# Kernel optimization log

Hardware: AMD Instinct MI355X
Metric: run time of the kernel (lower is better)

The kernel has to match this reference:

```python
import jax, jax.numpy as jnp
import numpy as np

B, T, E, H, V, D, C = 16384, 128, 32, 128, 30001, 128, 3


def setup_inputs() -> dict:
    key = jax.random.key(0)
    ks = jax.random.split(key, 8)
    tokens = jax.random.randint(ks[0], (B, T), 0, V, dtype=jnp.int32)
    emb = jax.random.normal(ks[1], (V, E), jnp.float32) * 0.05
    W = jax.random.normal(ks[2], (E, 3 * H), jnp.float32) * (1.0 / np.sqrt(E))
    U = jax.random.normal(ks[3], (H, 3 * H), jnp.float32) * (1.0 / np.sqrt(H))
    b = jnp.zeros((2, 3 * H), jnp.float32)  # [input_bias, recurrent_bias] (reset_after=True)
    W1 = jax.random.normal(ks[4], (H, D), jnp.float32) * (1.0 / np.sqrt(H))
    b1 = jnp.zeros((D,), jnp.float32)
    Wout = jax.random.normal(ks[5], (D, C), jnp.float32) * (1.0 / np.sqrt(D))
    bout = jnp.zeros((C,), jnp.float32)
    return {"tokens": tokens, "emb": emb, "W": W, "U": U, "b": b,
            "W1": W1, "b1": b1, "Wout": Wout, "bout": bout}


def _gru_masked(x, mask, W, U, b):
    # x: [B,T,E], mask: [B,T] bool. Keras GRU defaults: reset_after=True,
    # activation=tanh, recurrent_activation=sigmoid. Masked steps freeze state.
    xp = jnp.einsum('bte,eg->btg', x, W) + b[0]  # precompute input projections [B,T,3H]

    def step(h, inp):
        xg, m = inp                      # xg: [B,3H], m: [B]
        rec = h @ U + b[1]               # [B,3H]
        z = jax.nn.sigmoid(xg[:, :H] + rec[:, :H])
        r = jax.nn.sigmoid(xg[:, H:2 * H] + rec[:, H:2 * H])
        hh = jnp.tanh(xg[:, 2 * H:] + r * rec[:, 2 * H:])
        h_new = z * h + (1.0 - z) * hh
        h = jnp.where(m[:, None], h_new, h)
        return h, None

    h0 = jnp.zeros((x.shape[0], H), x.dtype)
    h, _ = jax.lax.scan(step, h0, (jnp.swapaxes(xp, 0, 1), jnp.swapaxes(mask, 0, 1)))
    return h


def reference(tokens, emb, W, U, b, W1, b1, Wout, bout):
    x = emb[tokens]                      # [B,T,E] embedding lookup
    mask = tokens != 0                   # mask_zero=True
    h = _gru_masked(x, mask, W, U, b)    # [B,H]
    d = h @ W1 + b1
    d = d * jax.nn.sigmoid(d)            # swish
    logits = d @ Wout + bout
    return jax.nn.softmax(logits, axis=-1)
```

## Files before the change

### kernel.cpp

```cpp
#include <hip/hip_runtime.h>
#include <hip/hip_fp16.h>

#define B_ 16384
#define T_ 128
#define E_ 32
#define H_ 128
#define G3_ 384
#define V_ 30001
#define D_ 128
#define C_ 3

#define LOG2E 1.44269504088896340736f

typedef _Float16 f16;
typedef f16 f16x4 __attribute__((ext_vector_type(4)));
typedef f16 f16x8 __attribute__((ext_vector_type(8)));
typedef float f32x4 __attribute__((ext_vector_type(4)));
typedef unsigned int u32;
typedef u32 u32x4 __attribute__((ext_vector_type(4)));

#define H0_OFF   0
#define H1_OFF   4096
#define TOK_OFF  8192
#define DBUF_OFF 16384
#define LDS_TOTAL 24832

__device__ __forceinline__ float frcp_(float x)  { return __builtin_amdgcn_rcpf(x); }
__device__ __forceinline__ float fexp2_(float x) { return __builtin_amdgcn_exp2f(x); }

#define K1_ROWS 8
__global__ __launch_bounds__(384) void embw_kernel(
    const float* __restrict__ emb,
    const float* __restrict__ W,
    const float* __restrict__ b_in,
    f16* __restrict__ embW)
{
    __shared__ float sW[E_][G3_];
    __shared__ float sE[K1_ROWS][E_];
    const int g = threadIdx.x;
    #pragma unroll
    for (int e = 0; e < E_; ++e) sW[e][g] = W[e * G3_ + g];
    const int v0 = blockIdx.x * K1_ROWS;
    for (int idx = g; idx < K1_ROWS * E_; idx += 384) {
        int rr = idx >> 5, ee = idx & 31;
        int v = v0 + rr;
        sE[rr][ee] = (v < V_) ? emb[v * E_ + ee] : 0.f;
    }
    __syncthreads();
    const float bg = b_in[g];
    const int c = g & 127, slot = g >> 7;
    const float sc = (slot == 2) ? (2.f * LOG2E) : (-LOG2E);
    #pragma unroll
    for (int rr = 0; rr < K1_ROWS; ++rr) {
        int v = v0 + rr;
        if (v >= V_) break;
        float acc = bg;
        #pragma unroll
        for (int e = 0; e < E_; ++e) acc = fmaf(sE[rr][e], sW[e][g], acc);
        embW[(size_t)v * 512 + c * 4 + slot] = (f16)(acc * sc);
    }
}

__global__ __launch_bounds__(512, 4) void gru_mfma_kernel(
    const int*   __restrict__ tokens,
    const f16*   __restrict__ embW,
    const float* __restrict__ U,
    const float* __restrict__ b,
    const float* __restrict__ W1,
    const float* __restrict__ b1,
    const float* __restrict__ Wout,
    const float* __restrict__ bout,
    float* __restrict__ out)
{
    __shared__ char lds[LDS_TOTAL];
    const int tid = threadIdx.x;
    const int w   = tid >> 6;
    const int l   = tid & 63;
    const int cl  = l & 15;
    const int q   = l >> 4;
    const int R0  = blockIdx.x * 16;
    const int col = w * 16 + cl;

    for (int idx = tid; idx < 16 * T_; idx += 512) {
        int r = idx >> 7, t = idx & 127;
        u32 tok = (u32)tokens[(size_t)(R0 + r) * T_ + t];
        *(u32*)(&lds[TOK_OFF + t * 64 + r * 4]) = tok * 1024u;
    }
    for (int idx = tid; idx < 1024; idx += 512)
        ((float*)(lds + H0_OFF))[idx] = 0.f;

    f16x8 Bf[3][4];
    #pragma unroll
    for (int gt = 0; gt < 3; ++gt) {
        const float sc = (gt == 2) ? (2.f * LOG2E) : (-LOG2E);
        const int n = gt * 128 + col;
        #pragma unroll
        for (int kt = 0; kt < 4; ++kt) {
            const int k0 = kt * 32 + q * 8;
            f16x8 fr;
            #pragma unroll
            for (int j = 0; j < 8; ++j)
                fr[j] = (f16)(U[(size_t)(k0 + j) * G3_ + n] * sc);
            Bf[gt][kt] = fr;
        }
    }

    const float bz = -LOG2E * b[G3_ + col];
    const float br = -LOG2E * b[G3_ + 128 + col];
    const float bh = 2.f * LOG2E * b[G3_ + 256 + col];

    float hreg[4];
    #pragma unroll
    for (int i = 0; i < 4; ++i) hreg[i] = 0.f;

    __syncthreads();

    const char* embWb = (const char*)embW;
    const int col8 = col * 8;

    u32x4 offc = *(const u32x4*)(&lds[TOK_OFF + q * 16]);
    f16x4 xvc[4];
    #pragma unroll
    for (int i = 0; i < 4; ++i)
        xvc[i] = *(const f16x4*)(embWb + offc[i] + col8);

    int cur = 0;
    for (int t = 0; t < T_; ++t) {
        const char* hb = lds + (cur ? H1_OFF : H0_OFF);
        char*       hn = lds + (cur ? H0_OFF : H1_OFF);

        u32x4 offn = offc;
        f16x4 xvn[4];
        #pragma unroll
        for (int i = 0; i < 4; ++i) xvn[i] = xvc[i];
        if (t + 1 < T_) {
            offn = *(const u32x4*)(&lds[TOK_OFF + (t + 1) * 64 + q * 16]);
            #pragma unroll
            for (int i = 0; i < 4; ++i)
                xvn[i] = *(const f16x4*)(embWb + offn[i] + col8);
        }

        f32x4 accz = {bz, bz, bz, bz};
        f32x4 accr = {br, br, br, br};
        f32x4 acch = {bh, bh, bh, bh};
        #pragma unroll
        for (int kt = 0; kt < 4; ++kt) {
            const int chunk = (kt * 64 + q * 16) ^ ((cl & 7) << 4);
            const f16x8 af = *(const f16x8*)(hb + cl * 256 + chunk);
            accz = __builtin_amdgcn_mfma_f32_16x16x32_f16(af, Bf[0][kt], accz, 0, 0, 0);
            accr = __builtin_amdgcn_mfma_f32_16x16x32_f16(af, Bf[1][kt], accr, 0, 0, 0);
            acch = __builtin_amdgcn_mfma_f32_16x16x32_f16(af, Bf[2][kt], acch, 0, 0, 0);
        }

        #pragma unroll
        for (int i = 0; i < 4; ++i) {
            const float z  = frcp_(1.f + fexp2_((float)xvc[i][0] + accz[i]));
            const float r  = frcp_(1.f + fexp2_((float)xvc[i][1] + accr[i]));
            const float hh = fmaf(-2.f, frcp_(1.f + fexp2_(fmaf(r, acch[i], (float)xvc[i][2]))), 1.f);
            const float hv = hreg[i];
            float nv = fmaf(z, hv - hh, hh);
            nv = (offc[i] != 0u) ? nv : hv;
            hreg[i] = nv;
            const int row = 4 * q + i;
            *(f16*)(hn + row * 256 + ((col * 2) ^ ((row & 7) << 4))) = (f16)nv;
        }
        __syncthreads();
        cur ^= 1;
        offc = offn;
        #pragma unroll
        for (int i = 0; i < 4; ++i) xvc[i] = xvn[i];
    }

    {
        f16x8 Wf[4];
        #pragma unroll
        for (int kt = 0; kt < 4; ++kt) {
            const int k0 = kt * 32 + q * 8;
            f16x8 fr;
            #pragma unroll
            for (int j = 0; j < 8; ++j)
                fr[j] = (f16)W1[(size_t)(k0 + j) * D_ + col];
            Wf[kt] = fr;
        }
        const char* hb = lds + H0_OFF;
        const float bd = b1[col];
        f32x4 dacc = {bd, bd, bd, bd};
        #pragma unroll
        for (int kt = 0; kt < 4; ++kt) {
            const int chunk = (kt * 64 + q * 16) ^ ((cl & 7) << 4);
            const f16x8 af = *(const f16x8*)(hb + cl * 256 + chunk);
            dacc = __builtin_amdgcn_mfma_f32_16x16x32_f16(af, Wf[kt], dacc, 0, 0, 0);
        }
        #pragma unroll
        for (int i = 0; i < 4; ++i) {
            const float v = dacc[i];
            const float sw = v * frcp_(1.f + fexp2_(-LOG2E * v));
            *(float*)(&lds[DBUF_OFF + (4 * q + i) * 528 + col * 4]) = sw;
        }
    }
    __syncthreads();

    if (w == 0 && l < 48) {
        const int row = l & 15, ci = l >> 4;
        float acc = bout[ci];
        #pragma unroll 4
        for (int k = 0; k < D_; ++k)
            acc = fmaf(*(const float*)(&lds[DBUF_OFF + row * 528 + k * 4]),
                       Wout[k * 3 + ci], acc);
        const float v0 = __shfl(acc, row);
        const float v1 = __shfl(acc, row + 16);
        const float v2 = __shfl(acc, row + 32);
        const float mx = fmaxf(v0, fmaxf(v1, v2));
        const float e0 = fexp2_(LOG2E * (v0 - mx));
        const float e1 = fexp2_(LOG2E * (v1 - mx));
        const float e2 = fexp2_(LOG2E * (v2 - mx));
        const float inv = frcp_(e0 + e1 + e2);
        const float mine = (ci == 0) ? e0 : (ci == 1) ? e1 : e2;
        out[(size_t)(R0 + row) * 3 + ci] = mine * inv;
    }
}

extern "C" void kernel_launch(void* const* d_in, const int* in_sizes, int n_in,
                              void* d_out, int out_size, void* d_ws, size_t ws_size,
                              hipStream_t stream) {
    (void)in_sizes; (void)n_in; (void)out_size; (void)ws_size;
    const int*   tokens = (const int*)d_in[0];
    const float* emb    = (const float*)d_in[1];
    const float* W      = (const float*)d_in[2];
    const float* U      = (const float*)d_in[3];
    const float* b      = (const float*)d_in[4];
    const float* W1     = (const float*)d_in[5];
    const float* b1     = (const float*)d_in[6];
    const float* Wout   = (const float*)d_in[7];
    const float* bout   = (const float*)d_in[8];
    float* out  = (float*)d_out;
    f16*   embW = (f16*)d_ws;

    hipLaunchKernelGGL(embw_kernel, dim3((V_ + K1_ROWS - 1) / K1_ROWS), dim3(384), 0, stream,
                       emb, W, b, embW);
    hipLaunchKernelGGL(gru_mfma_kernel, dim3(B_ / 16), dim3(512), 0, stream,
                       tokens, embW, U, b, W1, b1, Wout, bout, out);
}
```

Baseline: 375.7 us.

## Transpose recurrent MFMA so each lane owns one row with 4 contiguous columns

Swaps MFMA operand roles so U is the A operand and h is the B operand. Each lane then holds four consecutive hidden columns of a single batch row. This lets the mask come from one token per lane and lets the embedding projection be read as three contiguous f16x4 loads from a plain [V,384] layout. The hidden-state store becomes one f16x4 write per lane instead of four scalar f16 writes, and the XOR swizzle is replaced by a padded 272-byte row pitch. The per-step gather stays the same size, but it is now split into three separate 8-byte loads per lane, each at a different 256-byte offset.

```diff
diff --git a/kernel.cpp b/kernel.cpp
--- a/kernel.cpp
+++ b/kernel.cpp
@@ -17,13 +17,13 @@
 typedef f16 f16x8 __attribute__((ext_vector_type(8)));
 typedef float f32x4 __attribute__((ext_vector_type(4)));
 typedef unsigned int u32;
-typedef u32 u32x4 __attribute__((ext_vector_type(4)));
-
+
+#define HPITCH   272
 #define H0_OFF   0
-#define H1_OFF   4096
-#define TOK_OFF  8192
-#define DBUF_OFF 16384
-#define LDS_TOTAL 24832
+#define H1_OFF   4352
+#define TOK_OFF  8704
+#define DBUF_OFF 16896
+#define LDS_TOTAL 25344
 
 __device__ __forceinline__ float frcp_(float x)  { return __builtin_amdgcn_rcpf(x); }
 __device__ __forceinline__ float fexp2_(float x) { return __builtin_amdgcn_exp2f(x); }
@@ -48,8 +48,7 @@
     }
     __syncthreads();
     const float bg = b_in[g];
-    const int c = g & 127, slot = g >> 7;
-    const float sc = (slot == 2) ? (2.f * LOG2E) : (-LOG2E);
+    const float sc = (g >= 256) ? (2.f * LOG2E) : (-LOG2E);
     #pragma unroll
     for (int rr = 0; rr < K1_ROWS; ++rr) {
         int v = v0 + rr;
@@ -57,7 +56,7 @@
         float acc = bg;
         #pragma unroll
         for (int e = 0; e < E_; ++e) acc = fmaf(sE[rr][e], sW[e][g], acc);
-        embW[(size_t)v * 512 + c * 4 + slot] = (f16)(acc * sc);
+        embW[(size_t)v * G3_ + g] = (f16)(acc * sc);
     }
 }
 
@@ -79,21 +78,21 @@
     const int cl  = l & 15;
     const int q   = l >> 4;
     const int R0  = blockIdx.x * 16;
-    const int col = w * 16 + cl;
+    const int c0  = w * 16 + 4 * q;
 
     for (int idx = tid; idx < 16 * T_; idx += 512) {
         int r = idx >> 7, t = idx & 127;
         u32 tok = (u32)tokens[(size_t)(R0 + r) * T_ + t];
-        *(u32*)(&lds[TOK_OFF + t * 64 + r * 4]) = tok * 1024u;
-    }
-    for (int idx = tid; idx < 1024; idx += 512)
+        *(u32*)(&lds[TOK_OFF + t * 64 + r * 4]) = tok * 768u;
+    }
+    for (int idx = tid; idx < H1_OFF / 4; idx += 512)
         ((float*)(lds + H0_OFF))[idx] = 0.f;
 
-    f16x8 Bf[3][4];
+    f16x8 Af[3][4];
     #pragma unroll
     for (int gt = 0; gt < 3; ++gt) {
         const float sc = (gt == 2) ? (2.f * LOG2E) : (-LOG2E);
-        const int n = gt * 128 + col;
+        const int n = gt * 128 + w * 16 + cl;
         #pragma unroll
         for (int kt = 0; kt < 4; ++kt) {
             const int k0 = kt * 32 + q * 8;
@@ -101,13 +100,17 @@
             #pragma unroll
             for (int j = 0; j < 8; ++j)
                 fr[j] = (f16)(U[(size_t)(k0 + j) * G3_ + n] * sc);
-            Bf[gt][kt] = fr;
-        }
-    }
-
-    const float bz = -LOG2E * b[G3_ + col];
-    const float br = -LOG2E * b[G3_ + 128 + col];
-    const float bh = 2.f * LOG2E * b[G3_ + 256 + col];
+            Af[gt][kt] = fr;
+        }
+    }
+
+    f32x4 bz4, br4, bh4;
+    #pragma unroll
+    for (int i = 0; i < 4; ++i) {
+        bz4[i] = -LOG2E * b[G3_ + c0 + i];
+        br4[i] = -LOG2E * b[G3_ + 128 + c0 + i];
+        bh4[i] = 2.f * LOG2E * b[G3_ + 256 + c0 + i];
+    }
 
     float hreg[4];
     #pragma unroll
@@ -116,59 +119,61 @@
     __syncthreads();
 
     const char* embWb = (const char*)embW;
-    const int col8 = col * 8;
-
-    u32x4 offc = *(const u32x4*)(&lds[TOK_OFF + q * 16]);
-    f16x4 xvc[4];
-    #pragma unroll
-    for (int i = 0; i < 4; ++i)
-        xvc[i] = *(const f16x4*)(embWb + offc[i] + col8);
+    const int colb = c0 * 2;
+
+    u32 offc = *(const u32*)(&lds[TOK_OFF + cl * 4]);
+    f16x4 xzc = *(const f16x4*)(embWb + offc + colb);
+    f16x4 xrc = *(const f16x4*)(embWb + offc + colb + 256);
+    f16x4 xhc = *(const f16x4*)(embWb + offc + colb + 512);
 
     int cur = 0;
     for (int t = 0; t < T_; ++t) {
         const char* hb = lds + (cur ? H1_OFF : H0_OFF);
         char*       hn = lds + (cur ? H0_OFF : H1_OFF);
 
-        u32x4 offn = offc;
-        f16x4 xvn[4];
-        #pragma unroll
-        for (int i = 0; i < 4; ++i) xvn[i] = xvc[i];
+        u32 offn = offc;
+        f16x4 xzn = xzc, xrn = xrc, xhn = xhc;
         if (t + 1 < T_) {
-            offn = *(const u32x4*)(&lds[TOK_OFF + (t + 1) * 64 + q * 16]);
-            #pragma unroll
-            for (int i = 0; i < 4; ++i)
-                xvn[i] = *(const f16x4*)(embWb + offn[i] + col8);
-        }
-
-        f32x4 accz = {bz, bz, bz, bz};
-        f32x4 accr = {br, br, br, br};
-        f32x4 acch = {bh, bh, bh, bh};
-        #pragma unroll
-        for (int kt = 0; kt < 4; ++kt) {
-            const int chunk = (kt * 64 + q * 16) ^ ((cl & 7) << 4);
-            const f16x8 af = *(const f16x8*)(hb + cl * 256 + chunk);
-            accz = __builtin_amdgcn_mfma_f32_16x16x32_f16(af, Bf[0][kt], accz, 0, 0, 0);
-            accr = __builtin_amdgcn_mfma_f32_16x16x32_f16(af, Bf[1][kt], accr, 0, 0, 0);
-            acch = __builtin_amdgcn_mfma_f32_16x16x32_f16(af, Bf[2][kt], acch, 0, 0, 0);
-        }
-
+            offn = *(const u32*)(&lds[TOK_OFF + (t + 1) * 64 + cl * 4]);
+            xzn = *(const f16x4*)(embWb + offn + colb);
+            xrn = *(const f16x4*)(embWb + offn + colb + 256);
+            xhn = *(const f16x4*)(embWb + offn + colb + 512);
+        }
+
+        const f16x8 bf0 = *(const f16x8*)(hb + cl * HPITCH + q * 16);
+        const f16x8 bf1 = *(const f16x8*)(hb + cl * HPITCH + q * 16 + 64);
+        const f16x8 bf2 = *(const f16x8*)(hb + cl * HPITCH + q * 16 + 128);
+        const f16x8 bf3 = *(const f16x8*)(hb + cl * HPITCH + q * 16 + 192);
+        f32x4 accz = __builtin_amdgcn_mfma_f32_16x16x32_f16(Af[0][0], bf0, bz4, 0, 0, 0);
+        f32x4 accr = __builtin_amdgcn_mfma_f32_16x16x32_f16(Af[1][0], bf0, br4, 0, 0, 0);
+        f32x4 acch = __builtin_amdgcn_mfma_f32_16x16x32_f16(Af[2][0], bf0, bh4, 0, 0, 0);
+        accz = __builtin_amdgcn_mfma_f32_16x16x32_f16(Af[0][1], bf1, accz, 0, 0, 0);
+        accr = __builtin_amdgcn_mfma_f32_16x16x32_f16(Af[1][1], bf1, accr, 0, 0, 0);
+        acch = __builtin_amdgcn_mfma_f32_16x16x32_f16(Af[2][1], bf1, acch, 0, 0, 0);
+        accz = __builtin_amdgcn_mfma_f32_16x16x32_f16(Af[0][2], bf2, accz, 0, 0, 0);
+        accr = __builtin_amdgcn_mfma_f32_16x16x32_f16(Af[1][2], bf2, accr, 0, 0, 0);
+        acch = __builtin_amdgcn_mfma_f32_16x16x32_f16(Af[2][2], bf2, acch, 0, 0, 0);
+        accz = __builtin_amdgcn_mfma_f32_16x16x32_f16(Af[0][3], bf3, accz, 0, 0, 0);
+        accr = __builtin_amdgcn_mfma_f32_16x16x32_f16(Af[1][3], bf3, accr, 0, 0, 0);
+        acch = __builtin_amdgcn_mfma_f32_16x16x32_f16(Af[2][3], bf3, acch, 0, 0, 0);
+
+        f16x4 hv4;
         #pragma unroll
         for (int i = 0; i < 4; ++i) {
-            const float z  = frcp_(1.f + fexp2_((float)xvc[i][0] + accz[i]));
-            const float r  = frcp_(1.f + fexp2_((float)xvc[i][1] + accr[i]));
-            const float hh = fmaf(-2.f, frcp_(1.f + fexp2_(fmaf(r, acch[i], (float)xvc[i][2]))), 1.f);
+            const float z  = frcp_(1.f + fexp2_((float)xzc[i] + accz[i]));
+            const float r  = frcp_(1.f + fexp2_((float)xrc[i] + accr[i]));
+            const float hh = fmaf(-2.f, frcp_(1.f + fexp2_(fmaf(r, acch[i], (float)xhc[i]))), 1.f);
             const float hv = hreg[i];
             float nv = fmaf(z, hv - hh, hh);
-            nv = (offc[i] != 0u) ? nv : hv;
+            nv = (offc != 0u) ? nv : hv;
             hreg[i] = nv;
-            const int row = 4 * q + i;
-            *(f16*)(hn + row * 256 + ((col * 2) ^ ((row & 7) << 4))) = (f16)nv;
-        }
+            hv4[i] = (f16)nv;
+        }
+        *(f16x4*)(hn + cl * HPITCH + colb) = hv4;
+
         __syncthreads();
         cur ^= 1;
-        offc = offn;
-        #pragma unroll
-        for (int i = 0; i < 4; ++i) xvc[i] = xvn[i];
+        offc = offn; xzc = xzn; xrc = xrn; xhc = xhn;
     }
 
     {
@@ -179,24 +184,28 @@
             f16x8 fr;
             #pragma unroll
             for (int j = 0; j < 8; ++j)
-                fr[j] = (f16)W1[(size_t)(k0 + j) * D_ + col];
+                fr[j] = (f16)W1[(size_t)(k0 + j) * D_ + w * 16 + cl];
             Wf[kt] = fr;
         }
         const char* hb = lds + H0_OFF;
-        const float bd = b1[col];
-        f32x4 dacc = {bd, bd, bd, bd};
-        #pragma unroll
-        for (int kt = 0; kt < 4; ++kt) {
-            const int chunk = (kt * 64 + q * 16) ^ ((cl & 7) << 4);
-            const f16x8 af = *(const f16x8*)(hb + cl * 256 + chunk);
-            dacc = __builtin_amdgcn_mfma_f32_16x16x32_f16(af, Wf[kt], dacc, 0, 0, 0);
-        }
+        f32x4 bd4;
+        #pragma unroll
+        for (int i = 0; i < 4; ++i) bd4[i] = b1[c0 + i];
+        const f16x8 bf0 = *(const f16x8*)(hb + cl * HPITCH + q * 16);
+        const f16x8 bf1 = *(const f16x8*)(hb + cl * HPITCH + q * 16 + 64);
+        const f16x8 bf2 = *(const f16x8*)(hb + cl * HPITCH + q * 16 + 128);
+        const f16x8 bf3 = *(const f16x8*)(hb + cl * HPITCH + q * 16 + 192);
+        f32x4 dacc = __builtin_amdgcn_mfma_f32_16x16x32_f16(Wf[0], bf0, bd4, 0, 0, 0);
+        dacc = __builtin_amdgcn_mfma_f32_16x16x32_f16(Wf[1], bf1, dacc, 0, 0, 0);
+        dacc = __builtin_amdgcn_mfma_f32_16x16x32_f16(Wf[2], bf2, dacc, 0, 0, 0);
+        dacc = __builtin_amdgcn_mfma_f32_16x16x32_f16(Wf[3], bf3, dacc, 0, 0, 0);
+        f32x4 sw4;
         #pragma unroll
         for (int i = 0; i < 4; ++i) {
             const float v = dacc[i];
-            const float sw = v * frcp_(1.f + fexp2_(-LOG2E * v));
-            *(float*)(&lds[DBUF_OFF + (4 * q + i) * 528 + col * 4]) = sw;
-        }
+            sw4[i] = v * frcp_(1.f + fexp2_(-LOG2E * v));
+        }
+        *(f32x4*)(&lds[DBUF_OFF + cl * 528 + c0 * 4]) = sw4;
     }
     __syncthreads();
 
```

Result: slower. 395.4 us (+5.2%).

## Give each wave its own 16 batch rows, keeping U in LDS and dropping block barriers

Applied to the files above, without the earlier changes.

Previously a 512-thread block of 8 waves split the 384 gate columns for 16 rows and synchronized every timestep. Now each block holds U transposed in LDS and runs 4 independent waves. Each wave handles 16 rows and all gate columns, so the per-step __syncthreads is gone. The r/z recurrent biases are folded into the precomputed embedding projection, whose layout is rearranged to match the new per-lane accumulator order. In exchange, U is reloaded from LDS every step, which means much more LDS traffic, and occupancy falls to one 256-thread block per CU with a large LDS footprint.

```diff
diff --git a/kernel.cpp b/kernel.cpp
--- a/kernel.cpp
+++ b/kernel.cpp
@@ -17,13 +17,13 @@
 typedef f16 f16x8 __attribute__((ext_vector_type(8)));
 typedef float f32x4 __attribute__((ext_vector_type(4)));
 typedef unsigned int u32;
-typedef u32 u32x4 __attribute__((ext_vector_type(4)));
-
-#define H0_OFF   0
-#define H1_OFF   4096
-#define TOK_OFF  8192
-#define DBUF_OFF 16384
-#define LDS_TOTAL 24832
+
+#define UTPITCH   272
+#define UT_BYTES  (G3_ * UTPITCH)
+#define SLAB_SZ   12608
+#define HS_OFF    0
+#define TK_OFF    4352
+#define LDS_TOTAL (UT_BYTES + 4 * SLAB_SZ)
 
 __device__ __forceinline__ float frcp_(float x)  { return __builtin_amdgcn_rcpf(x); }
 __device__ __forceinline__ float fexp2_(float x) { return __builtin_amdgcn_exp2f(x); }
@@ -32,7 +32,7 @@
 __global__ __launch_bounds__(384) void embw_kernel(
     const float* __restrict__ emb,
     const float* __restrict__ W,
-    const float* __restrict__ b_in,
+    const float* __restrict__ b,
     f16* __restrict__ embW)
 {
     __shared__ float sW[E_][G3_];
@@ -47,9 +47,11 @@
         sE[rr][ee] = (v < V_) ? emb[v * E_ + ee] : 0.f;
     }
     __syncthreads();
-    const float bg = b_in[g];
-    const int c = g & 127, slot = g >> 7;
-    const float sc = (slot == 2) ? (2.f * LOG2E) : (-LOG2E);
+    const float bg = b[g] + ((g < 256) ? b[G3_ + g] : 0.f);
+    const float sc = (g >= 256) ? (2.f * LOG2E) : (-LOG2E);
+    const int slot = g >> 7, c = g & 127;
+    const int t8 = c >> 4, q = (c >> 2) & 3, i = c & 3;
+    const int pos = ((slot * 4 + q) * 8 + t8) * 4 + i;
     #pragma unroll
     for (int rr = 0; rr < K1_ROWS; ++rr) {
         int v = v0 + rr;
@@ -57,11 +59,11 @@
         float acc = bg;
         #pragma unroll
         for (int e = 0; e < E_; ++e) acc = fmaf(sE[rr][e], sW[e][g], acc);
-        embW[(size_t)v * 512 + c * 4 + slot] = (f16)(acc * sc);
+        embW[(size_t)v * G3_ + pos] = (f16)(acc * sc);
     }
 }
 
-__global__ __launch_bounds__(512, 4) void gru_mfma_kernel(
+__global__ __launch_bounds__(256, 1) void gru_mfma_kernel(
     const int*   __restrict__ tokens,
     const f16*   __restrict__ embW,
     const float* __restrict__ U,
@@ -78,135 +80,149 @@
     const int l   = tid & 63;
     const int cl  = l & 15;
     const int q   = l >> 4;
-    const int R0  = blockIdx.x * 16;
-    const int col = w * 16 + cl;
-
-    for (int idx = tid; idx < 16 * T_; idx += 512) {
-        int r = idx >> 7, t = idx & 127;
-        u32 tok = (u32)tokens[(size_t)(R0 + r) * T_ + t];
-        *(u32*)(&lds[TOK_OFF + t * 64 + r * 4]) = tok * 1024u;
-    }
-    for (int idx = tid; idx < 1024; idx += 512)
-        ((float*)(lds + H0_OFF))[idx] = 0.f;
-
-    f16x8 Bf[3][4];
-    #pragma unroll
-    for (int gt = 0; gt < 3; ++gt) {
-        const float sc = (gt == 2) ? (2.f * LOG2E) : (-LOG2E);
-        const int n = gt * 128 + col;
-        #pragma unroll
-        for (int kt = 0; kt < 4; ++kt) {
-            const int k0 = kt * 32 + q * 8;
-            f16x8 fr;
-            #pragma unroll
-            for (int j = 0; j < 8; ++j)
-                fr[j] = (f16)(U[(size_t)(k0 + j) * G3_ + n] * sc);
-            Bf[gt][kt] = fr;
+    const int R0  = blockIdx.x * 64;
+
+    for (int idx = tid; idx < G3_ * H_; idx += 256) {
+        const int c = idx % G3_, k = idx / G3_;
+        const float sc = (c >= 256) ? (2.f * LOG2E) : (-LOG2E);
+        *(f16*)(&lds[c * UTPITCH + k * 2]) = (f16)(U[(size_t)k * G3_ + c] * sc);
+    }
+    for (int idx = tid; idx < 64 * T_; idx += 256) {
+        const int r = idx >> 7, t = idx & 127;
+        const u32 tok = (u32)tokens[(size_t)(R0 + r) * T_ + t];
+        *(u32*)(&lds[UT_BYTES + (r >> 4) * SLAB_SZ + TK_OFF + t * 64 + (r & 15) * 4])
+            = tok * 768u;
+    }
+    if (tid < 64)
+        *(u32*)(&lds[UT_BYTES + (tid >> 4) * SLAB_SZ + TK_OFF + 128 * 64 + (tid & 15) * 4]) = 0u;
+    for (int idx = tid; idx < 4 * 1088; idx += 256)
+        *(float*)(&lds[UT_BYTES + (idx / 1088) * SLAB_SZ + HS_OFF + (idx % 1088) * 4]) = 0.f;
+
+    __syncthreads();
+
+    char* slab  = &lds[UT_BYTES + w * SLAB_SZ];
+    char* hs    = slab + HS_OFF;
+    const char* tokp = slab + TK_OFF;
+    const char* embWb = (const char*)embW;
+
+    f32x4 bhr[8];
+    #pragma unroll
+    for (int t8 = 0; t8 < 8; ++t8)
+        #pragma unroll
+        for (int i = 0; i < 4; ++i)
+            bhr[t8][i] = 2.f * LOG2E * b[G3_ + 256 + 16 * t8 + 4 * q + i];
+
+    float hreg[8][4];
+    #pragma unroll
+    for (int t8 = 0; t8 < 8; ++t8)
+        #pragma unroll
+        for (int i = 0; i < 4; ++i) hreg[t8][i] = 0.f;
+
+    u32 offc = *(const u32*)(tokp + cl * 4);
+    f16x8 xgC[3][4];
+    #pragma unroll
+    for (int s = 0; s < 3; ++s) {
+        const char* p = embWb + offc + ((s * 4 + q) << 6);
+        #pragma unroll
+        for (int u = 0; u < 4; ++u) xgC[s][u] = *(const f16x8*)(p + u * 16);
+    }
+
+    for (int t = 0; t < T_; ++t) {
+        f16x8 bf[4];
+        #pragma unroll
+        for (int kt = 0; kt < 4; ++kt)
+            bf[kt] = *(const f16x8*)(hs + cl * UTPITCH + kt * 64 + q * 16);
+
+        const u32 offn = *(const u32*)(tokp + (t + 1) * 64 + cl * 4);
+        f16x8 xgN[3][4];
+        #pragma unroll
+        for (int s = 0; s < 3; ++s) {
+            const char* p = embWb + offn + ((s * 4 + q) << 6);
+            #pragma unroll
+            for (int u = 0; u < 4; ++u) xgN[s][u] = *(const f16x8*)(p + u * 16);
         }
-    }
-
-    const float bz = -LOG2E * b[G3_ + col];
-    const float br = -LOG2E * b[G3_ + 128 + col];
-    const float bh = 2.f * LOG2E * b[G3_ + 256 + col];
-
-    float hreg[4];
-    #pragma unroll
-    for (int i = 0; i < 4; ++i) hreg[i] = 0.f;
-
-    __syncthreads();
-
-    const char* embWb = (const char*)embW;
-    const int col8 = col * 8;
-
-    u32x4 offc = *(const u32x4*)(&lds[TOK_OFF + q * 16]);
-    f16x4 xvc[4];
-    #pragma unroll
-    for (int i = 0; i < 4; ++i)
-        xvc[i] = *(const f16x4*)(embWb + offc[i] + col8);
-
-    int cur = 0;
-    for (int t = 0; t < T_; ++t) {
-        const char* hb = lds + (cur ? H1_OFF : H0_OFF);
-        char*       hn = lds + (cur ? H0_OFF : H1_OFF);
-
-        u32x4 offn = offc;
-        f16x4 xvn[4];
-        #pragma unroll
-        for (int i = 0; i < 4; ++i) xvn[i] = xvc[i];
-        if (t + 1 < T_) {
-            offn = *(const u32x4*)(&lds[TOK_OFF + (t + 1) * 64 + q * 16]);
-            #pragma unroll
-            for (int i = 0; i < 4; ++i)
-                xvn[i] = *(const f16x4*)(embWb + offn[i] + col8);
+
+        const int abase = cl * UTPITCH + q * 16;
+
+        #pragma unroll
+        for (int t8 = 0; t8 < 8; ++t8) {
+            const int u = t8 >> 1, hh4 = (t8 & 1) << 2;
+            f32x4 az, ar;
+            #pragma unroll
+            for (int i = 0; i < 4; ++i) {
+                az[i] = (float)xgC[0][u][hh4 + i];
+                ar[i] = (float)xgC[1][u][hh4 + i];
+            }
+            f32x4 ah = bhr[t8];
+            #pragma unroll
+            for (int kt = 0; kt < 4; ++kt) {
+                const f16x8 afz = *(const f16x8*)(&lds[(0 * 128 + 16 * t8) * UTPITCH + abase + kt * 64]);
+                const f16x8 afr = *(const f16x8*)(&lds[(1 * 128 + 16 * t8) * UTPITCH + abase + kt * 64]);
+                const f16x8 afh = *(const f16x8*)(&lds[(2 * 128 + 16 * t8) * UTPITCH + abase + kt * 64]);
+                az = __builtin_amdgcn_mfma_f32_16x16x32_f16(afz, bf[kt], az, 0, 0, 0);
+                ar = __builtin_amdgcn_mfma_f32_16x16x32_f16(afr, bf[kt], ar, 0, 0, 0);
+                ah = __builtin_amdgcn_mfma_f32_16x16x32_f16(afh, bf[kt], ah, 0, 0, 0);
+            }
+            f16x4 hv4;
+            #pragma unroll
+            for (int i = 0; i < 4; ++i) {
+                const float z  = frcp_(1.f + fexp2_(az[i]));
+                const float r  = frcp_(1.f + fexp2_(ar[i]));
+                const float xh = (float)xgC[2][u][hh4 + i];
+                const float hh = fmaf(-2.f, frcp_(1.f + fexp2_(fmaf(r, ah[i], xh))), 1.f);
+                const float hv = hreg[t8][i];
+                float nv = fmaf(z, hv - hh, hh);
+                nv = (offc != 0u) ? nv : hv;
+                hreg[t8][i] = nv;
+                hv4[i] = (f16)nv;
+            }
+            *(f16x4*)(hs + cl * UTPITCH + t8 * 32 + q * 8) = hv4;
         }
 
-        f32x4 accz = {bz, bz, bz, bz};
-        f32x4 accr = {br, br, br, br};
-        f32x4 acch = {bh, bh, bh, bh};
-        #pragma unroll
-        for (int kt = 0; kt < 4; ++kt) {
-            const int chunk = (kt * 64 + q * 16) ^ ((cl & 7) << 4);
-            const f16x8 af = *(const f16x8*)(hb + cl * 256 + chunk);
-            accz = __builtin_amdgcn_mfma_f32_16x16x32_f16(af, Bf[0][kt], accz, 0, 0, 0);
-            accr = __builtin_amdgcn_mfma_f32_16x16x32_f16(af, Bf[1][kt], accr, 0, 0, 0);
-            acch = __builtin_amdgcn_mfma_f32_16x16x32_f16(af, Bf[2][kt], acch, 0, 0, 0);
+        offc = offn;
+        #pragma unroll
+        for (int s = 0; s < 3; ++s)
+            #pragma unroll
+            for (int u = 0; u < 4; ++u) xgC[s][u] = xgN[s][u];
+    }
+
+    {
+        f16x8 bf[4];
+        #pragma unroll
+        for (int kt = 0; kt < 4; ++kt)
+            bf[kt] = *(const f16x8*)(hs + cl * UTPITCH + kt * 64 + q * 16);
+        asm volatile("s_waitcnt lgkmcnt(0)" ::: "memory");
+
+        #pragma unroll
+        for (int t8 = 0; t8 < 8; ++t8) {
+            f32x4 dacc;
+            #pragma unroll
+            for (int i = 0; i < 4; ++i) dacc[i] = b1[16 * t8 + 4 * q + i];
+            #pragma unroll
+            for (int kt = 0; kt < 4; ++kt) {
+                f16x8 wf;
+                #pragma unroll
+                for (int j = 0; j < 8; ++j)
+                    wf[j] = (f16)W1[(size_t)(kt * 32 + q * 8 + j) * D_ + 16 * t8 + cl];
+                dacc = __builtin_amdgcn_mfma_f32_16x16x32_f16(wf, bf[kt], dacc, 0, 0, 0);
+            }
+            f32x4 sw;
+            #pragma unroll
+            for (int i = 0; i < 4; ++i) {
+                const float v = dacc[i];
+                sw[i] = v * frcp_(1.f + fexp2_(-LOG2E * v));
+            }
+            *(f32x4*)(slab + cl * 528 + (16 * t8 + 4 * q) * 4) = sw;
         }
-
-        #pragma unroll
-        for (int i = 0; i < 4; ++i) {
-            const float z  = frcp_(1.f + fexp2_((float)xvc[i][0] + accz[i]));
-            const float r  = frcp_(1.f + fexp2_((float)xvc[i][1] + accr[i]));
-            const float hh = fmaf(-2.f, frcp_(1.f + fexp2_(fmaf(r, acch[i], (float)xvc[i][2]))), 1.f);
-            const float hv = hreg[i];
-            float nv = fmaf(z, hv - hh, hh);
-            nv = (offc[i] != 0u) ? nv : hv;
-            hreg[i] = nv;
-            const int row = 4 * q + i;
-            *(f16*)(hn + row * 256 + ((col * 2) ^ ((row & 7) << 4))) = (f16)nv;
-        }
-        __syncthreads();
-        cur ^= 1;
-        offc = offn;
-        #pragma unroll
-        for (int i = 0; i < 4; ++i) xvc[i] = xvn[i];
-    }
-
-    {
-        f16x8 Wf[4];
-        #pragma unroll
-        for (int kt = 0; kt < 4; ++kt) {
-            const int k0 = kt * 32 + q * 8;
-            f16x8 fr;
-            #pragma unroll
-            for (int j = 0; j < 8; ++j)
-                fr[j] = (f16)W1[(size_t)(k0 + j) * D_ + col];
-            Wf[kt] = fr;
-        }
-        const char* hb = lds + H0_OFF;
-        const float bd = b1[col];
-        f32x4 dacc = {bd, bd, bd, bd};
-        #pragma unroll
-        for (int kt = 0; kt < 4; ++kt) {
-            const int chunk = (kt * 64 + q * 16) ^ ((cl & 7) << 4);
-            const f16x8 af = *(const f16x8*)(hb + cl * 256 + chunk);
-            dacc = __builtin_amdgcn_mfma_f32_16x16x32_f16(af, Wf[kt], dacc, 0, 0, 0);
-        }
-        #pragma unroll
-        for (int i = 0; i < 4; ++i) {
-            const float v = dacc[i];
-            const float sw = v * frcp_(1.f + fexp2_(-LOG2E * v));
-            *(float*)(&lds[DBUF_OFF + (4 * q + i) * 528 + col * 4]) = sw;
-        }
-    }
-    __syncthreads();
-
-    if (w == 0 && l < 48) {
+        asm volatile("s_waitcnt lgkmcnt(0)" ::: "memory");
+    }
+
+    if (l < 48) {
         const int row = l & 15, ci = l >> 4;
         float acc = bout[ci];
         #pragma unroll 4
         for (int k = 0; k < D_; ++k)
-            acc = fmaf(*(const float*)(&lds[DBUF_OFF + row * 528 + k * 4]),
-                       Wout[k * 3 + ci], acc);
+            acc = fmaf(*(const float*)(slab + row * 528 + k * 4), Wout[k * 3 + ci], acc);
         const float v0 = __shfl(acc, row);
         const float v1 = __shfl(acc, row + 16);
         const float v2 = __shfl(acc, row + 32);
@@ -216,7 +232,7 @@
         const float e2 = fexp2_(LOG2E * (v2 - mx));
         const float inv = frcp_(e0 + e1 + e2);
         const float mine = (ci == 0) ? e0 : (ci == 1) ? e1 : e2;
-        out[(size_t)(R0 + row) * 3 + ci] = mine * inv;
+        out[(size_t)(R0 + w * 16 + row) * 3 + ci] = mine * inv;
     }
 }
 
@@ -238,6 +254,6 @@
 
     hipLaunchKernelGGL(embw_kernel, dim3((V_ + K1_ROWS - 1) / K1_ROWS), dim3(384), 0, stream,
                        emb, W, b, embW);
-    hipLaunchKernelGGL(gru_mfma_kernel, dim3(B_ / 16), dim3(512), 0, stream,
+    hipLaunchKernelGGL(gru_mfma_kernel, dim3(B_ / 64), dim3(256), 0, stream,
                        tokens, embW, U, b, W1, b1, Wout, bout, out);
 }
```

Result: slower. 494.6 us (+31.7%).
